# Kernel tuning notes

Measured on AMD Instinct MI355X. Metric: run time of the kernel, lower is better.

Reference implementation:

```python
import jax, jax.numpy as jnp
import numpy as np
from jax.scipy.special import logsumexp

DIM_N, DIM_E, DIM_U = 64, 128, 64
MID, A = 32, 16
N_PER, B = 12, 128  # 128 fully-connected graphs of 12 nodes


def _lin_params(k, fin, fout):
    k1, k2 = jax.random.split(k)
    lim = 1.0 / np.sqrt(fin)
    W = jax.random.uniform(k1, (fin, fout), minval=-lim, maxval=lim)
    b = jax.random.uniform(k2, (fout,), minval=-lim, maxval=lim)
    return W, b


def setup_inputs() -> dict:
    key = jax.random.key(0)
    ks = jax.random.split(key, 12)
    # fully connected directed graph (no self loops), per component
    s, d = np.meshgrid(np.arange(N_PER), np.arange(N_PER), indexing='ij')
    m = s != d
    s1, d1 = s[m].astype(np.int64), d[m].astype(np.int64)
    Epg = s1.size  # 132
    M = np.zeros((N_PER, N_PER), np.int64)
    M[s1, d1] = np.arange(Epg)
    rev1 = M[d1, s1]
    noff = (np.arange(B, dtype=np.int64) * N_PER)[:, None]
    eoff = (np.arange(B, dtype=np.int64) * Epg)[:, None]
    src = jnp.asarray((s1[None] + noff).reshape(-1))
    dst = jnp.asarray((d1[None] + noff).reshape(-1))
    idx_revs = jnp.asarray((rev1[None] + eoff).reshape(-1))
    E, Nt = B * Epg, B * N_PER
    edge_feats = jax.random.normal(ks[0], (E, DIM_E))
    node_feats = jax.random.normal(ks[1], (Nt, DIM_N))
    graph_feats = jax.random.normal(ks[2], (B, DIM_U))
    edge_feat_reflected = edge_feats[idx_revs]
    u = jax.random.uniform(ks[3], (E, 2), minval=1e-6, maxval=1.0)
    gumbel_noise = -jnp.log(-jnp.log(u))
    W_jf, b_jf = _lin_params(ks[4], DIM_E + DIM_U, A * MID)
    W_if, b_if = _lin_params(ks[5], DIM_N + DIM_U, A)
    W_ju, b_ju = _lin_params(ks[6], DIM_E + DIM_U, A * MID)
    W_iu, b_iu = _lin_params(ks[7], DIM_N + DIM_U, A)
    W_fl, b_fl = _lin_params(ks[8], DIM_E + DIM_U, MID)
    W_cls, b_cls = _lin_params(ks[9], MID, 2)
    return dict(edge_feats=edge_feats, node_feats=node_feats, graph_feats=graph_feats,
                edge_feat_reflected=edge_feat_reflected, src=src, dst=dst, idx_revs=idx_revs,
                gumbel_noise=gumbel_noise, W_jf=W_jf, b_jf=b_jf, W_if=W_if, b_if=b_if,
                W_ju=W_ju, b_ju=b_ju, W_iu=W_iu, b_iu=b_iu, W_fl=W_fl, b_fl=b_fl,
                W_cls=W_cls, b_cls=b_cls)


def reference(edge_feats, node_feats, graph_feats, edge_feat_reflected, src, dst, idx_revs,
              gumbel_noise, W_jf, b_jf, W_if, b_if, W_ju, b_ju, W_iu, b_iu,
              W_fl, b_fl, W_cls, b_cls):
    Bn = graph_feats.shape[0]
    Nt = node_feats.shape[0]
    E = edge_feats.shape[0]
    npg = Nt // Bn          # nodes per graph == number of BP iterations
    epg = E // Bn
    a = b_if.shape[0]       # num_acts
    mid = W_cls.shape[0]    # mid_pair

    # broadcast graph-level features to edges / nodes
    u_e = jnp.repeat(graph_feats, epg, axis=0)   # [E, du]
    u_n = jnp.repeat(graph_feats, npg, axis=0)   # [Nt, du]

    xe = jnp.concatenate([edge_feats, u_e], axis=-1)
    xer = jnp.concatenate([edge_feat_reflected, u_e], axis=-1)
    xn = jnp.concatenate([node_feats, u_n], axis=-1)

    indiv_factor = xn @ W_if + b_if      # [Nt, A]
    indiv_util = xn @ W_iu + b_iu        # [Nt, A]

    fc = (xe @ W_jf + b_jf).reshape(E, a, mid)
    fcr = (xer @ W_jf + b_jf).reshape(E, a, mid)
    factor_vals = jnp.einsum('eam,ebm->eab', fc, fcr)   # [E, A, A]
    uc = (xe @ W_ju + b_ju).reshape(E, a, mid)
    ucr = (xer @ W_ju + b_ju).reshape(E, a, mid)
    util_vals = jnp.einsum('eam,ebm->eab', uc, ucr)     # [E, A, A]

    # hard gumbel-softmax edge gating; noise shared with reverse edge
    flag_repr = (xe @ W_fl + b_fl) * (xer @ W_fl + b_fl)
    logits = flag_repr @ W_cls + b_cls                  # [E, 2]
    eid = jnp.arange(E)
    noise = gumbel_noise[jnp.minimum(eid, idx_revs)]
    y_soft = jax.nn.softmax(logits + noise, axis=-1)
    y_hard = jax.nn.one_hot(jnp.argmax(y_soft, axis=-1), 2, dtype=y_soft.dtype)
    flags = y_soft + jax.lax.stop_gradient(y_hard - y_soft)
    flag0 = flags[:, 0][:, None]                        # [E, 1]

    fvT = factor_vals.transpose(0, 2, 1)
    uvT = util_vals.transpose(0, 2, 1)
    if_src, if_dst = indiv_factor[src], indiv_factor[dst]
    iu_src, iu_dst = indiv_util[src], indiv_util[dst]

    def step(carry, _):
        mm_n, um_n, msg_e, rmsg_e, umsg_e, rumsg_e = carry
        agg = mm_n[src] - rmsg_e + if_src                      # [E, A]
        m = factor_vals + agg[:, None, :]                      # [E, A, A]
        m_sum = jax.nn.log_softmax(logsumexp(m, axis=-1), axis=-1)
        new_msg = m_sum * flag0
        agg_rev = mm_n[dst] - msg_e + if_dst
        m_rev = fvT + agg_rev[:, None, :]
        m_rev_sum = jax.nn.log_softmax(logsumexp(m_rev, axis=-1), axis=-1)
        new_rmsg = m_rev_sum * flag0
        util = um_n[src] - rumsg_e + iu_src
        new_umsg = ((util_vals + util[:, None, :]) * jax.nn.softmax(m, axis=-1)).sum(-1) * flag0
        rev_util = um_n[dst] - umsg_e + iu_dst
        new_rumsg = ((uvT + rev_util[:, None, :]) * jax.nn.softmax(m_rev, axis=-1)).sum(-1) * flag0
        new_mm_n = jax.ops.segment_sum(new_msg, dst, num_segments=Nt)
        new_um_n = jax.ops.segment_sum(new_umsg, dst, num_segments=Nt)
        return (new_mm_n, new_um_n, new_msg, new_rmsg, new_umsg, new_rumsg), None

    zn = jnp.zeros((Nt, a), edge_feats.dtype)
    ze = jnp.zeros((E, a), edge_feats.dtype)
    carry0 = (zn, zn, ze, ze, ze, ze)
    (mm_n, um_n, _, _, _, _), _ = jax.lax.scan(step, carry0, None, length=npg)

    node0 = jnp.arange(Bn) * npg
    return (um_n + indiv_util)[node0]   # [B, A]
```

## Files before the change

kernel.cpp:

```cpp
#include <hip/hip_runtime.h>
#include <hip/hip_bf16.h>

typedef unsigned short ushort_t;
typedef __bf16 bf16x8 __attribute__((ext_vector_type(8)));
typedef float f32x4 __attribute__((ext_vector_type(4)));

#define E_TOT 16896
#define NT    1536
#define BGR   128
#define NPG   12
#define EPG   132
#define KD    192
#define KD2   576
#define NJ    512
#define ADIM  16
#define MIDD  32
#define NCAN  8448

#if defined(__has_builtin)
#  if __has_builtin(__builtin_amdgcn_global_load_lds)
#    define HAS_GLL 1
#  else
#    define HAS_GLL 0
#  endif
#else
#  define HAS_GLL 0
#endif

#if HAS_GLL
__device__ __forceinline__ void gll16(const ushort_t* g, ushort_t* s) {
    __builtin_amdgcn_global_load_lds(
        (const __attribute__((address_space(1))) unsigned int*)g,
        (__attribute__((address_space(3))) unsigned int*)s, 16, 0, 0);
}
#endif

__device__ __forceinline__ float b2f(ushort_t u) {
    union { float f; unsigned int i; } c; c.i = ((unsigned int)u) << 16; return c.f;
}
__device__ __forceinline__ ushort_t f2b(float f) {
    union { float f; unsigned int i; } c; c.f = f;
    unsigned int i = c.i;
    unsigned int r = (i + 0x7FFFu + ((i >> 16) & 1u)) >> 16;
    return (ushort_t)r;
}
__device__ __forceinline__ int rev_local(int i) {
    int s = i / 11;
    int p = i - 11 * s;
    int d = p + (p >= s ? 1 : 0);
    return d * 11 + (s < d ? s : s - 1);
}

__global__ __launch_bounds__(256) void prep_kernel(
    const float* __restrict__ Wjf, const float* __restrict__ Wju,
    const float* __restrict__ ef,  const float* __restrict__ gf,
    ushort_t* __restrict__ WtJFs, ushort_t* __restrict__ WtJUs,
    ushort_t* __restrict__ XeS)
{
    int idx = blockIdx.x * 256 + threadIdx.x;
    const int T1 = NJ * KD;
    if (idx < T1) {
        int n = idx / KD, k = idx - n * KD;
        float wf = Wjf[k * NJ + n];
        ushort_t hf = f2b(wf);
        WtJFs[n * KD2 + k]       = hf;
        WtJFs[n * KD2 + 192 + k] = hf;
        WtJFs[n * KD2 + 384 + k] = f2b(wf - b2f(hf));
        float wu = Wju[k * NJ + n];
        ushort_t hu = f2b(wu);
        WtJUs[n * KD2 + k]       = hu;
        WtJUs[n * KD2 + 192 + k] = hu;
        WtJUs[n * KD2 + 384 + k] = f2b(wu - b2f(hu));
        return;
    }
    idx -= T1;
    if (idx < E_TOT * KD) {
        int e = idx / KD, k = idx - e * KD;
        float x = (k < 128) ? ef[(size_t)e * 128 + k] : gf[(e / EPG) * 64 + (k - 128)];
        ushort_t h = f2b(x);
        XeS[(size_t)e * KD2 + k]       = h;
        XeS[(size_t)e * KD2 + 192 + k] = f2b(x - b2f(h));
        XeS[(size_t)e * KD2 + 384 + k] = h;
    }
}

__global__ __launch_bounds__(256) void gemm_kernel(
    const ushort_t* __restrict__ X, const ushort_t* __restrict__ Wt,
    const float* __restrict__ bias, float* __restrict__ H)
{
    __shared__ ushort_t As[2][128][32];
    __shared__ ushort_t Bs[2][128][32];
    int tid = threadIdx.x, lane = tid & 63, w = tid >> 6;
    int m0 = blockIdx.y * 128, n0 = blockIdx.x * 128;
    int wm = (w >> 1) * 64, wn = (w & 1) * 64;
    int r = lane & 15, q = lane >> 4;
    f32x4 acc[4][4] = {};

    int sr = w * 32 + (lane >> 2);
    int sc = (lane & 3) * 8;
    const ushort_t* xg0 = X  + (size_t)(m0 + sr)      * KD2 + sc;
    const ushort_t* xg1 = X  + (size_t)(m0 + sr + 16) * KD2 + sc;
    const ushort_t* wg0 = Wt + (size_t)(n0 + sr)      * KD2 + sc;
    const ushort_t* wg1 = Wt + (size_t)(n0 + sr + 16) * KD2 + sc;

#if HAS_GLL
    auto stage = [&](int p, int kk) {
        gll16(xg0 + kk, &As[p][w * 32][0]);
        gll16(xg1 + kk, &As[p][w * 32 + 16][0]);
        gll16(wg0 + kk, &Bs[p][w * 32][0]);
        gll16(wg1 + kk, &Bs[p][w * 32 + 16][0]);
    };
#else
    auto stage = [&](int p, int kk) {
        uint4 a0 = *(const uint4*)(xg0 + kk);
        uint4 a1 = *(const uint4*)(xg1 + kk);
        uint4 b0 = *(const uint4*)(wg0 + kk);
        uint4 b1 = *(const uint4*)(wg1 + kk);
        *(uint4*)&As[p][sr][sc]      = a0;
        *(uint4*)&As[p][sr + 16][sc] = a1;
        *(uint4*)&Bs[p][sr][sc]      = b0;
        *(uint4*)&Bs[p][sr + 16][sc] = b1;
    };
#endif

    stage(0, 0);
    int cur = 0;
    for (int kk = 0; kk < KD2; kk += 32) {
        __syncthreads();
        if (kk + 32 < KD2) stage(cur ^ 1, kk + 32);
        bf16x8 af[4], bf[4];
#pragma unroll
        for (int mi = 0; mi < 4; ++mi)
            af[mi] = *(const bf16x8*)&As[cur][wm + mi * 16 + r][q * 8];
#pragma unroll
        for (int ni = 0; ni < 4; ++ni)
            bf[ni] = *(const bf16x8*)&Bs[cur][wn + ni * 16 + r][q * 8];
#pragma unroll
        for (int mi = 0; mi < 4; ++mi)
#pragma unroll
            for (int ni = 0; ni < 4; ++ni)
                acc[mi][ni] = __builtin_amdgcn_mfma_f32_16x16x32_bf16(
                    af[mi], bf[ni], acc[mi][ni], 0, 0, 0);
        cur ^= 1;
    }
#pragma unroll
    for (int ni = 0; ni < 4; ++ni) {
        int col = n0 + wn + ni * 16 + r;
        float bvf = bias[col];
#pragma unroll
        for (int mi = 0; mi < 4; ++mi) {
            int rowb = m0 + wm + mi * 16 + q * 4;
            float* dst = H + (size_t)rowb * NJ + col;
#pragma unroll
            for (int rr = 0; rr < 4; ++rr)
                dst[(size_t)rr * NJ] = acc[mi][ni][rr] + bvf;
        }
    }
}

__global__ __launch_bounds__(256) void pair_kernel(
    const float* __restrict__ H, float* __restrict__ OutV)
{
    __shared__ float sA[4][16][36];
    __shared__ float sB[4][16][36];
    __shared__ float sC[4][16][20];
    int tid = threadIdx.x, w = tid >> 6, lane = tid & 63;
    int c = blockIdx.x * 4 + w;
    int gg = c / 66, cl = c - gg * 66;
    int s = 0;
    while (cl >= 11 - s) { cl -= 11 - s; ++s; }
    int d = s + 1 + cl;
    int e  = gg * EPG + s * 11 + (d - 1);
    int re = gg * EPG + d * 11 + s;
    const float* hA = H + (size_t)e * NJ;
    const float* hB = H + (size_t)re * NJ;
    int a = lane >> 2, mseg = (lane & 3) * 8;
    float4 va0 = *(const float4*)(hA + a * 32 + mseg);
    float4 va1 = *(const float4*)(hA + a * 32 + mseg + 4);
    float4 vb0 = *(const float4*)(hB + a * 32 + mseg);
    float4 vb1 = *(const float4*)(hB + a * 32 + mseg + 4);
    *(float4*)&sA[w][a][mseg]     = va0;
    *(float4*)&sA[w][a][mseg + 4] = va1;
    *(float4*)&sB[w][a][mseg]     = vb0;
    *(float4*)&sB[w][a][mseg + 4] = vb1;
    __syncthreads();

    int b = lane & 15, a0 = (lane >> 4) * 4;
    float4 ac0 = {0,0,0,0}, ac1 = {0,0,0,0}, ac2 = {0,0,0,0}, ac3 = {0,0,0,0};
#pragma unroll
    for (int m4 = 0; m4 < 8; ++m4) {
        float4 vb = *(const float4*)&sB[w][b][m4 * 4];
        float4 x0 = *(const float4*)&sA[w][a0 + 0][m4 * 4];
        float4 x1 = *(const float4*)&sA[w][a0 + 1][m4 * 4];
        float4 x2 = *(const float4*)&sA[w][a0 + 2][m4 * 4];
        float4 x3 = *(const float4*)&sA[w][a0 + 3][m4 * 4];
        ac0.x += x0.x * vb.x; ac0.y += x0.y * vb.y; ac0.z += x0.z * vb.z; ac0.w += x0.w * vb.w;
        ac1.x += x1.x * vb.x; ac1.y += x1.y * vb.y; ac1.z += x1.z * vb.z; ac1.w += x1.w * vb.w;
        ac2.x += x2.x * vb.x; ac2.y += x2.y * vb.y; ac2.z += x2.z * vb.z; ac2.w += x2.w * vb.w;
        ac3.x += x3.x * vb.x; ac3.y += x3.y * vb.y; ac3.z += x3.z * vb.z; ac3.w += x3.w * vb.w;
    }
    float v0 = ac0.x + ac0.y + ac0.z + ac0.w;
    float v1 = ac1.x + ac1.y + ac1.z + ac1.w;
    float v2 = ac2.x + ac2.y + ac2.z + ac2.w;
    float v3 = ac3.x + ac3.y + ac3.z + ac3.w;
    float* oe = OutV + (size_t)e * 256;
    oe[(a0 + 0) * 16 + b] = v0;
    oe[(a0 + 1) * 16 + b] = v1;
    oe[(a0 + 2) * 16 + b] = v2;
    oe[(a0 + 3) * 16 + b] = v3;
    sC[w][b][a0 + 0] = v0;
    sC[w][b][a0 + 1] = v1;
    sC[w][b][a0 + 2] = v2;
    sC[w][b][a0 + 3] = v3;
    __syncthreads();
    int rr = lane >> 2, cc = (lane & 3) * 4;
    float4 t4 = { sC[w][rr][cc], sC[w][rr][cc + 1], sC[w][rr][cc + 2], sC[w][rr][cc + 3] };
    *(float4*)(OutV + (size_t)re * 256 + lane * 4) = t4;
}

__global__ __launch_bounds__(256) void hfl_kernel(
    const float* __restrict__ ef, const float* __restrict__ gf,
    const float* __restrict__ Wfl, const float* __restrict__ bfl,
    float* __restrict__ HFL)
{
    __shared__ float Ws[KD][32];
    __shared__ float xr[64][KD];
    int tid = threadIdx.x;
    int e0 = blockIdx.x * 64;
    for (int i = tid; i < KD * 32; i += 256) Ws[i >> 5][i & 31] = Wfl[i];
    for (int i4 = tid; i4 < 64 * 48; i4 += 256) {
        int slot = i4 / 48, kq = i4 - slot * 48;
        int e = e0 + slot;
        float4 v;
        if (kq < 32) v = *(const float4*)&ef[(size_t)e * 128 + kq * 4];
        else         v = *(const float4*)&gf[(e / EPG) * 64 + (kq - 32) * 4];
        *(float4*)&xr[slot][kq * 4] = v;
    }
    __syncthreads();
    int j = tid & 31, es = tid >> 5;
    float acc[8];
#pragma unroll
    for (int i = 0; i < 8; ++i) acc[i] = bfl[j];
    for (int k = 0; k < KD; k += 4) {
        float w0 = Ws[k][j], w1 = Ws[k + 1][j], w2 = Ws[k + 2][j], w3 = Ws[k + 3][j];
#pragma unroll
        for (int i = 0; i < 8; ++i) {
            float4 x4 = *(const float4*)&xr[es + 8 * i][k];
            acc[i] += x4.x * w0; acc[i] += x4.y * w1;
            acc[i] += x4.z * w2; acc[i] += x4.w * w3;
        }
    }
#pragma unroll
    for (int i = 0; i < 8; ++i)
        HFL[(size_t)(e0 + es + 8 * i) * 32 + j] = acc[i];
}

__global__ __launch_bounds__(256) void node_kernel(
    const float* __restrict__ nf, const float* __restrict__ gf,
    const float* __restrict__ Wif, const float* __restrict__ bif,
    const float* __restrict__ Wiu, const float* __restrict__ biu,
    float* __restrict__ IFF, float* __restrict__ IUU)
{
    __shared__ float Ws[128 * 32];
    __shared__ float xr[8][128];
    int tid = threadIdx.x;
    int n0 = blockIdx.x * 8;
    for (int i = tid; i < 128 * 32; i += 256) {
        int k = i >> 5, j = i & 31;
        Ws[i] = (j < 16) ? Wif[k * 16 + j] : Wiu[k * 16 + (j - 16)];
    }
    for (int i = tid; i < 8 * 128; i += 256) {
        int slot = i >> 7, k = i & 127;
        int n = n0 + slot;
        xr[slot][k] = (k < 64) ? nf[(size_t)n * 64 + k] : gf[(n / NPG) * 64 + (k - 64)];
    }
    __syncthreads();
    int slot = tid >> 5, j = tid & 31;
    float acc = (j < 16) ? bif[j] : biu[j - 16];
#pragma unroll 8
    for (int k = 0; k < 128; ++k) acc += xr[slot][k] * Ws[k * 32 + j];
    int n = n0 + slot;
    if (j < 16) IFF[n * 16 + j] = acc;
    else        IUU[n * 16 + (j - 16)] = acc;
}

__global__ __launch_bounds__(256) void flags_kernel(
    const float* __restrict__ HFL,
    const float* __restrict__ Wcls, const float* __restrict__ bcls,
    const float* __restrict__ gum, float* __restrict__ FL)
{
    int e = blockIdx.x * 256 + threadIdx.x;
    if (e >= E_TOT) return;
    int g = e / EPG, li = e - g * EPG;
    int re = g * EPG + rev_local(li);
    float l0 = bcls[0], l1 = bcls[1];
    const float* ha = HFL + (size_t)e * 32;
    const float* hb = HFL + (size_t)re * 32;
#pragma unroll
    for (int j = 0; j < 32; ++j) {
        float p = ha[j] * hb[j];
        l0 += p * Wcls[j * 2 + 0];
        l1 += p * Wcls[j * 2 + 1];
    }
    int mn = min(e, re);
    l0 += gum[(size_t)mn * 2 + 0];
    l1 += gum[(size_t)mn * 2 + 1];
    FL[e] = (l0 >= l1) ? 1.0f : 0.0f;
}

__global__ __launch_bounds__(704, 3) void bp_kernel(
    const float* __restrict__ FV, const float* __restrict__ UV,
    const float* __restrict__ FL, const float* __restrict__ IFF,
    const float* __restrict__ IUU, float* __restrict__ out)
{
    int g = blockIdx.x, tid = threadIdx.x;
    __shared__ float msg[2][EPG][16];
    __shared__ float umsg[2][EPG][16];
    __shared__ float Asum[NPG][16], Usum[NPG][16];
    __shared__ float iffs[NPG][16], iuus[NPG][16];
    __shared__ float fls[EPG];

    for (int i = tid; i < 2 * EPG * 16; i += 704) {
        (&msg[0][0][0])[i] = 0.f;
        (&umsg[0][0][0])[i] = 0.f;
    }
    for (int i = tid; i < NPG * 16; i += 704) {
        float fi = IFF[g * NPG * 16 + i];
        float ui = IUU[g * NPG * 16 + i];
        (&iffs[0][0])[i] = fi; (&iuus[0][0])[i] = ui;
        (&Asum[0][0])[i] = fi; (&Usum[0][0])[i] = ui;
    }
    for (int i = tid; i < EPG; i += 704) fls[i] = FL[g * EPG + i];

    int w44 = tid >> 4, a = tid & 15;
    int sidx[3], ridx[3], eidx[3];
    float fv[3][16], uv[3][16], fle[3];
    const float* fvg = FV + (size_t)g * EPG * 256;
    const float* uvg = UV + (size_t)g * EPG * 256;
#pragma unroll
    for (int j = 0; j < 3; ++j) {
        int e = j * 44 + w44;
        eidx[j] = e;
        sidx[j] = e / 11;
        ridx[j] = rev_local(e);
        const float* fr = fvg + (size_t)e * 256 + a * 16;
        const float* ur = uvg + (size_t)e * 256 + a * 16;
#pragma unroll
        for (int q = 0; q < 4; ++q) {
            float4 f4 = *(const float4*)(fr + q * 4);
            float4 u4 = *(const float4*)(ur + q * 4);
            fv[j][q * 4 + 0] = f4.x; fv[j][q * 4 + 1] = f4.y;
            fv[j][q * 4 + 2] = f4.z; fv[j][q * 4 + 3] = f4.w;
            uv[j][q * 4 + 0] = u4.x; uv[j][q * 4 + 1] = u4.y;
            uv[j][q * 4 + 2] = u4.z; uv[j][q * 4 + 3] = u4.w;
        }
    }
    __syncthreads();
#pragma unroll
    for (int j = 0; j < 3; ++j) fle[j] = fls[eidx[j]];

    int cur = 0;
    for (int it = 0; it < NPG; ++it) {
        int nxt = cur ^ 1;
#pragma unroll
        for (int j = 0; j < 3; ++j) {
            int e = eidx[j], s = sidx[j], re = ridx[j];
            float t_m[16], t_u[16];
#pragma unroll
            for (int q = 0; q < 4; ++q) {
                float4 av  = *(const float4*)&Asum[s][q * 4];
                float4 mv  = *(const float4*)&msg[cur][re][q * 4];
                float4 usv = *(const float4*)&Usum[s][q * 4];
                float4 umv = *(const float4*)&umsg[cur][re][q * 4];
                t_m[q * 4 + 0] = fv[j][q * 4 + 0] + (av.x - mv.x);
                t_m[q * 4 + 1] = fv[j][q * 4 + 1] + (av.y - mv.y);
                t_m[q * 4 + 2] = fv[j][q * 4 + 2] + (av.z - mv.z);
                t_m[q * 4 + 3] = fv[j][q * 4 + 3] + (av.w - mv.w);
                t_u[q * 4 + 0] = uv[j][q * 4 + 0] + (usv.x - umv.x);
                t_u[q * 4 + 1] = uv[j][q * 4 + 1] + (usv.y - umv.y);
                t_u[q * 4 + 2] = uv[j][q * 4 + 2] + (usv.z - umv.z);
                t_u[q * 4 + 3] = uv[j][q * 4 + 3] + (usv.w - umv.w);
            }
            float mx = t_m[0];
#pragma unroll
            for (int b = 1; b < 16; ++b) mx = fmaxf(mx, t_m[b]);
            float S = 0.f, num = 0.f;
#pragma unroll
            for (int b = 0; b < 16; ++b) {
                float ev = __expf(t_m[b] - mx);
                S += ev;
                num += t_u[b] * ev;
            }
            float lse = mx + __logf(S);
            float unv = num / S;
            float M2 = lse;
            M2 = fmaxf(M2, __shfl_xor(M2, 1));
            M2 = fmaxf(M2, __shfl_xor(M2, 2));
            M2 = fmaxf(M2, __shfl_xor(M2, 4));
            M2 = fmaxf(M2, __shfl_xor(M2, 8));
            float se = __expf(lse - M2);
            se += __shfl_xor(se, 1);
            se += __shfl_xor(se, 2);
            se += __shfl_xor(se, 4);
            se += __shfl_xor(se, 8);
            float LSE = M2 + __logf(se);
            msg[nxt][e][a] = (lse - LSE) * fle[j];
            umsg[nxt][e][a] = unv * fle[j];
        }
        __syncthreads();
        if (tid < NPG * 16) {
            int n = tid >> 4, aa = tid & 15;
            float sm = 0.f, su = 0.f;
#pragma unroll
            for (int s = 0; s < NPG; ++s) {
                if (s == n) continue;
                int le = s * 11 + (n < s ? n : n - 1);
                sm += msg[nxt][le][aa];
                su += umsg[nxt][le][aa];
            }
            Asum[n][aa] = sm + iffs[n][aa];
            Usum[n][aa] = su + iuus[n][aa];
        }
        __syncthreads();
        cur = nxt;
    }
    if (tid < 16) {
        out[g * 16 + tid] = Usum[0][tid];
    }
}

extern "C" void kernel_launch(void* const* d_in, const int* in_sizes, int n_in,
                              void* d_out, int out_size, void* d_ws, size_t ws_size,
                              hipStream_t stream) {
    const float* edge_feats  = (const float*)d_in[0];
    const float* node_feats  = (const float*)d_in[1];
    const float* graph_feats = (const float*)d_in[2];
    const float* gumbel      = (const float*)d_in[7];
    const float* W_jf        = (const float*)d_in[8];
    const float* b_jf        = (const float*)d_in[9];
    const float* W_if        = (const float*)d_in[10];
    const float* b_if        = (const float*)d_in[11];
    const float* W_ju        = (const float*)d_in[12];
    const float* b_ju        = (const float*)d_in[13];
    const float* W_iu        = (const float*)d_in[14];
    const float* b_iu        = (const float*)d_in[15];
    const float* W_fl        = (const float*)d_in[16];
    const float* b_fl        = (const float*)d_in[17];
    const float* W_cls       = (const float*)d_in[18];
    const float* b_cls       = (const float*)d_in[19];
    float* out = (float*)d_out;
    (void)in_sizes; (void)n_in; (void)out_size; (void)ws_size;

    size_t off = 0;
    char* base = (char*)d_ws;
    auto alloc = [&](size_t bytes) {
        void* p = base + off;
        off += (bytes + 255) & ~(size_t)255;
        return p;
    };
    ushort_t* XeS   = (ushort_t*)alloc((size_t)E_TOT * KD2 * 2);
    ushort_t* WtJFs = (ushort_t*)alloc((size_t)NJ * KD2 * 2);
    ushort_t* WtJUs = (ushort_t*)alloc((size_t)NJ * KD2 * 2);
    float*    Hbuf  = (float*)   alloc((size_t)E_TOT * NJ * 4);
    float*    FVv   = (float*)   alloc((size_t)E_TOT * 256 * 4);
    float*    FLG   = (float*)   alloc((size_t)E_TOT * 4);
    float*    IFFp  = (float*)   alloc((size_t)NT * 16 * 4);
    float*    IUUp  = (float*)   alloc((size_t)NT * 16 * 4);
    float* HFL = Hbuf;
    float* UVv = (float*)XeS;

    const int prep_blocks = (NJ * KD + E_TOT * KD) / 256;
    prep_kernel<<<prep_blocks, 256, 0, stream>>>(W_jf, W_ju, edge_feats, graph_feats,
                                                 WtJFs, WtJUs, XeS);
    node_kernel<<<NT / 8, 256, 0, stream>>>(node_feats, graph_feats, W_if, b_if,
                                            W_iu, b_iu, IFFp, IUUp);
    hfl_kernel<<<E_TOT / 64, 256, 0, stream>>>(edge_feats, graph_feats, W_fl, b_fl, HFL);
    flags_kernel<<<E_TOT / 256, 256, 0, stream>>>(HFL, W_cls, b_cls, gumbel, FLG);
    gemm_kernel<<<dim3(NJ / 128, E_TOT / 128), 256, 0, stream>>>(XeS, WtJFs, b_jf, Hbuf);
    pair_kernel<<<NCAN / 4, 256, 0, stream>>>(Hbuf, FVv);
    gemm_kernel<<<dim3(NJ / 128, E_TOT / 128), 256, 0, stream>>>(XeS, WtJUs, b_ju, Hbuf);
    pair_kernel<<<NCAN / 4, 256, 0, stream>>>(Hbuf, UVv);
    bp_kernel<<<BGR, 704, 0, stream>>>(FVv, UVv, FLG, IFFp, IUUp, out);
}
```

Before: 247.5 us.

## Batch both factor GEMMs and pair passes via grid z, fold node and flag kernels into bp

Merges the two edge-factor GEMMs and the two pair transforms into single launches indexed by a grid z/y dimension, writing to separate H and FV/UV buffers when the workspace is large enough. The node linear layers and the Gumbel flag classifier are computed inside the belief-propagation kernel's prologue instead of in separate kernels. This cuts four kernel launches and gives the GEMM twice as many blocks for better occupancy. In exchange it needs a larger workspace, and the node matmul now runs serially per thread inside bp_kernel.

```diff
diff --git a/kernel.cpp b/kernel.cpp
--- a/kernel.cpp
+++ b/kernel.cpp
@@ -85,11 +85,18 @@
 }
 
 __global__ __launch_bounds__(256) void gemm_kernel(
-    const ushort_t* __restrict__ X, const ushort_t* __restrict__ Wt,
-    const float* __restrict__ bias, float* __restrict__ H)
+    const ushort_t* __restrict__ X,
+    const ushort_t* __restrict__ Wt0, const ushort_t* __restrict__ Wt1,
+    const float* __restrict__ b0, const float* __restrict__ b1,
+    float* __restrict__ Hbase)
 {
     __shared__ ushort_t As[2][128][32];
     __shared__ ushort_t Bs[2][128][32];
+    int z = blockIdx.z;
+    const ushort_t* Wt = z ? Wt1 : Wt0;
+    const float* bias = z ? b1 : b0;
+    float* H = Hbase + (size_t)z * E_TOT * NJ;
+
     int tid = threadIdx.x, lane = tid & 63, w = tid >> 6;
     int m0 = blockIdx.y * 128, n0 = blockIdx.x * 128;
     int wm = (w >> 1) * 64, wn = (w & 1) * 64;
@@ -114,12 +121,12 @@
     auto stage = [&](int p, int kk) {
         uint4 a0 = *(const uint4*)(xg0 + kk);
         uint4 a1 = *(const uint4*)(xg1 + kk);
-        uint4 b0 = *(const uint4*)(wg0 + kk);
-        uint4 b1 = *(const uint4*)(wg1 + kk);
+        uint4 bb0 = *(const uint4*)(wg0 + kk);
+        uint4 bb1 = *(const uint4*)(wg1 + kk);
         *(uint4*)&As[p][sr][sc]      = a0;
         *(uint4*)&As[p][sr + 16][sc] = a1;
-        *(uint4*)&Bs[p][sr][sc]      = b0;
-        *(uint4*)&Bs[p][sr + 16][sc] = b1;
+        *(uint4*)&Bs[p][sr][sc]      = bb0;
+        *(uint4*)&Bs[p][sr + 16][sc] = bb1;
     };
 #endif
 
@@ -159,11 +166,13 @@
 }
 
 __global__ __launch_bounds__(256) void pair_kernel(
-    const float* __restrict__ H, float* __restrict__ OutV)
+    const float* __restrict__ Hbase, float* __restrict__ Obase)
 {
     __shared__ float sA[4][16][36];
     __shared__ float sB[4][16][36];
     __shared__ float sC[4][16][20];
+    const float* H = Hbase + (size_t)blockIdx.y * E_TOT * NJ;
+    float* OutV = Obase + (size_t)blockIdx.y * E_TOT * 256;
     int tid = threadIdx.x, w = tid >> 6, lane = tid & 63;
     int c = blockIdx.x * 4 + w;
     int gg = c / 66, cl = c - gg * 66;
@@ -255,63 +264,14 @@
         HFL[(size_t)(e0 + es + 8 * i) * 32 + j] = acc[i];
 }
 
-__global__ __launch_bounds__(256) void node_kernel(
+__global__ __launch_bounds__(704, 3) void bp_kernel(
+    const float* __restrict__ FV, const float* __restrict__ UV,
+    const float* __restrict__ HFL, const float* __restrict__ Wcls,
+    const float* __restrict__ bcls, const float* __restrict__ gum,
     const float* __restrict__ nf, const float* __restrict__ gf,
     const float* __restrict__ Wif, const float* __restrict__ bif,
     const float* __restrict__ Wiu, const float* __restrict__ biu,
-    float* __restrict__ IFF, float* __restrict__ IUU)
-{
-    __shared__ float Ws[128 * 32];
-    __shared__ float xr[8][128];
-    int tid = threadIdx.x;
-    int n0 = blockIdx.x * 8;
-    for (int i = tid; i < 128 * 32; i += 256) {
-        int k = i >> 5, j = i & 31;
-        Ws[i] = (j < 16) ? Wif[k * 16 + j] : Wiu[k * 16 + (j - 16)];
-    }
-    for (int i = tid; i < 8 * 128; i += 256) {
-        int slot = i >> 7, k = i & 127;
-        int n = n0 + slot;
-        xr[slot][k] = (k < 64) ? nf[(size_t)n * 64 + k] : gf[(n / NPG) * 64 + (k - 64)];
-    }
-    __syncthreads();
-    int slot = tid >> 5, j = tid & 31;
-    float acc = (j < 16) ? bif[j] : biu[j - 16];
-#pragma unroll 8
-    for (int k = 0; k < 128; ++k) acc += xr[slot][k] * Ws[k * 32 + j];
-    int n = n0 + slot;
-    if (j < 16) IFF[n * 16 + j] = acc;
-    else        IUU[n * 16 + (j - 16)] = acc;
-}
-
-__global__ __launch_bounds__(256) void flags_kernel(
-    const float* __restrict__ HFL,
-    const float* __restrict__ Wcls, const float* __restrict__ bcls,
-    const float* __restrict__ gum, float* __restrict__ FL)
-{
-    int e = blockIdx.x * 256 + threadIdx.x;
-    if (e >= E_TOT) return;
-    int g = e / EPG, li = e - g * EPG;
-    int re = g * EPG + rev_local(li);
-    float l0 = bcls[0], l1 = bcls[1];
-    const float* ha = HFL + (size_t)e * 32;
-    const float* hb = HFL + (size_t)re * 32;
-#pragma unroll
-    for (int j = 0; j < 32; ++j) {
-        float p = ha[j] * hb[j];
-        l0 += p * Wcls[j * 2 + 0];
-        l1 += p * Wcls[j * 2 + 1];
-    }
-    int mn = min(e, re);
-    l0 += gum[(size_t)mn * 2 + 0];
-    l1 += gum[(size_t)mn * 2 + 1];
-    FL[e] = (l0 >= l1) ? 1.0f : 0.0f;
-}
-
-__global__ __launch_bounds__(704, 3) void bp_kernel(
-    const float* __restrict__ FV, const float* __restrict__ UV,
-    const float* __restrict__ FL, const float* __restrict__ IFF,
-    const float* __restrict__ IUU, float* __restrict__ out)
+    float* __restrict__ out)
 {
     int g = blockIdx.x, tid = threadIdx.x;
     __shared__ float msg[2][EPG][16];
@@ -324,13 +284,35 @@
         (&msg[0][0][0])[i] = 0.f;
         (&umsg[0][0][0])[i] = 0.f;
     }
-    for (int i = tid; i < NPG * 16; i += 704) {
-        float fi = IFF[g * NPG * 16 + i];
-        float ui = IUU[g * NPG * 16 + i];
-        (&iffs[0][0])[i] = fi; (&iuus[0][0])[i] = ui;
-        (&Asum[0][0])[i] = fi; (&Usum[0][0])[i] = ui;
-    }
-    for (int i = tid; i < EPG; i += 704) fls[i] = FL[g * EPG + i];
+    if (tid < NPG * 16) {
+        int nl = tid >> 4, aa = tid & 15;
+        int n = g * NPG + nl;
+        float accf = bif[aa], accu = biu[aa];
+        for (int k = 0; k < 128; ++k) {
+            float x = (k < 64) ? nf[(size_t)n * 64 + k] : gf[g * 64 + (k - 64)];
+            accf += x * Wif[k * 16 + aa];
+            accu += x * Wiu[k * 16 + aa];
+        }
+        iffs[nl][aa] = accf; iuus[nl][aa] = accu;
+        Asum[nl][aa] = accf; Usum[nl][aa] = accu;
+    }
+    if (tid < EPG) {
+        int el = tid, rel = rev_local(el);
+        int e = g * EPG + el, re = g * EPG + rel;
+        float l0 = bcls[0], l1 = bcls[1];
+        const float* ha = HFL + (size_t)e * 32;
+        const float* hb = HFL + (size_t)re * 32;
+#pragma unroll
+        for (int j = 0; j < 32; ++j) {
+            float p = ha[j] * hb[j];
+            l0 += p * Wcls[j * 2 + 0];
+            l1 += p * Wcls[j * 2 + 1];
+        }
+        int mn = min(e, re);
+        l0 += gum[(size_t)mn * 2 + 0];
+        l1 += gum[(size_t)mn * 2 + 1];
+        fls[el] = (l0 >= l1) ? 1.0f : 0.0f;
+    }
 
     int w44 = tid >> 4, a = tid & 15;
     int sidx[3], ridx[3], eidx[3];
@@ -449,7 +431,7 @@
     const float* W_cls       = (const float*)d_in[18];
     const float* b_cls       = (const float*)d_in[19];
     float* out = (float*)d_out;
-    (void)in_sizes; (void)n_in; (void)out_size; (void)ws_size;
+    (void)in_sizes; (void)n_in; (void)out_size;
 
     size_t off = 0;
     char* base = (char*)d_ws;
@@ -461,24 +443,40 @@
     ushort_t* XeS   = (ushort_t*)alloc((size_t)E_TOT * KD2 * 2);
     ushort_t* WtJFs = (ushort_t*)alloc((size_t)NJ * KD2 * 2);
     ushort_t* WtJUs = (ushort_t*)alloc((size_t)NJ * KD2 * 2);
-    float*    Hbuf  = (float*)   alloc((size_t)E_TOT * NJ * 4);
-    float*    FVv   = (float*)   alloc((size_t)E_TOT * 256 * 4);
-    float*    FLG   = (float*)   alloc((size_t)E_TOT * 4);
-    float*    IFFp  = (float*)   alloc((size_t)NT * 16 * 4);
-    float*    IUUp  = (float*)   alloc((size_t)NT * 16 * 4);
-    float* HFL = Hbuf;
-    float* UVv = (float*)XeS;
-
+    float*    HFL   = (float*)   alloc((size_t)E_TOT * 32 * 4);
+
+    const size_t fused_need = off + (size_t)E_TOT * NJ * 2 * 4
+                                  + (size_t)E_TOT * 512 * 4
+                                  + 4096;
     const int prep_blocks = (NJ * KD + E_TOT * KD) / 256;
+
     prep_kernel<<<prep_blocks, 256, 0, stream>>>(W_jf, W_ju, edge_feats, graph_feats,
                                                  WtJFs, WtJUs, XeS);
-    node_kernel<<<NT / 8, 256, 0, stream>>>(node_feats, graph_feats, W_if, b_if,
-                                            W_iu, b_iu, IFFp, IUUp);
     hfl_kernel<<<E_TOT / 64, 256, 0, stream>>>(edge_feats, graph_feats, W_fl, b_fl, HFL);
-    flags_kernel<<<E_TOT / 256, 256, 0, stream>>>(HFL, W_cls, b_cls, gumbel, FLG);
-    gemm_kernel<<<dim3(NJ / 128, E_TOT / 128), 256, 0, stream>>>(XeS, WtJFs, b_jf, Hbuf);
-    pair_kernel<<<NCAN / 4, 256, 0, stream>>>(Hbuf, FVv);
-    gemm_kernel<<<dim3(NJ / 128, E_TOT / 128), 256, 0, stream>>>(XeS, WtJUs, b_ju, Hbuf);
-    pair_kernel<<<NCAN / 4, 256, 0, stream>>>(Hbuf, UVv);
-    bp_kernel<<<BGR, 704, 0, stream>>>(FVv, UVv, FLG, IFFp, IUUp, out);
-}
+
+    if (ws_size >= fused_need) {
+        float* H2   = (float*)alloc((size_t)E_TOT * NJ * 2 * 4);
+        float* FVUV = (float*)alloc((size_t)E_TOT * 512 * 4);
+        float* FVv = FVUV;
+        float* UVv = FVUV + (size_t)E_TOT * 256;
+        gemm_kernel<<<dim3(NJ / 128, E_TOT / 128, 2), 256, 0, stream>>>(
+            XeS, WtJFs, WtJUs, b_jf, b_ju, H2);
+        pair_kernel<<<dim3(NCAN / 4, 2), 256, 0, stream>>>(H2, FVUV);
+        bp_kernel<<<BGR, 704, 0, stream>>>(FVv, UVv, HFL, W_cls, b_cls, gumbel,
+                                           node_feats, graph_feats,
+                                           W_if, b_if, W_iu, b_iu, out);
+    } else {
+        float* Hbuf = (float*)alloc((size_t)E_TOT * NJ * 4);
+        float* FVv  = (float*)alloc((size_t)E_TOT * 256 * 4);
+        float* UVv  = (float*)XeS;
+        gemm_kernel<<<dim3(NJ / 128, E_TOT / 128, 1), 256, 0, stream>>>(
+            XeS, WtJFs, WtJFs, b_jf, b_jf, Hbuf);
+        pair_kernel<<<dim3(NCAN / 4, 1), 256, 0, stream>>>(Hbuf, FVv);
+        gemm_kernel<<<dim3(NJ / 128, E_TOT / 128, 1), 256, 0, stream>>>(
+            XeS, WtJUs, WtJUs, b_ju, b_ju, Hbuf);
+        pair_kernel<<<dim3(NCAN / 4, 1), 256, 0, stream>>>(Hbuf, UVv);
+        bp_kernel<<<BGR, 704, 0, stream>>>(FVv, UVv, HFL, W_cls, b_cls, gumbel,
+                                           node_feats, graph_feats,
+                                           W_if, b_if, W_iu, b_iu, out);
+    }
+}
```

After: 240.7 us. 1.03x faster.

## Fuse GEMM with pair contraction and fold node/flag kernels into neighbors

Applied to the files above, without the earlier changes.

The two big GEMMs and their pair contractions are merged into one kernel. Each block computes the full 512-wide H rows for 16 edge/reverse-edge pairs in shared memory and contracts them directly, so the large fp32 H intermediate never goes through global memory. The node projection is folded into the prep kernel as extra blocks, and the flag computation is moved into the BP kernel prologue, removing three launches. The cost is that each block now streams the whole weight matrix for only 32 rows, which cuts B-operand reuse, and the shared-memory footprint is larger, which may reduce occupancy.

```diff
diff --git a/kernel.cpp b/kernel.cpp
--- a/kernel.cpp
+++ b/kernel.cpp
@@ -13,9 +13,8 @@
 #define KD    192
 #define KD2   576
 #define NJ    512
-#define ADIM  16
-#define MIDD  32
 #define NCAN  8448
+#define PPB   16
 
 #if defined(__has_builtin)
 #  if __has_builtin(__builtin_amdgcn_global_load_lds)
@@ -50,76 +49,130 @@
     int d = p + (p >= s ? 1 : 0);
     return d * 11 + (s < d ? s : s - 1);
 }
+__device__ __forceinline__ void canon_decode(int c, int& e, int& re) {
+    int g = c / 66, cl = c - g * 66;
+    int s = 0;
+    while (cl >= 11 - s) { cl -= 11 - s; ++s; }
+    int d = s + 1 + cl;
+    e  = g * EPG + s * 11 + (d - 1);
+    re = g * EPG + d * 11 + s;
+}
 
 __global__ __launch_bounds__(256) void prep_kernel(
     const float* __restrict__ Wjf, const float* __restrict__ Wju,
     const float* __restrict__ ef,  const float* __restrict__ gf,
+    const float* __restrict__ nf,
+    const float* __restrict__ Wif, const float* __restrict__ bif,
+    const float* __restrict__ Wiu, const float* __restrict__ biu,
     ushort_t* __restrict__ WtJFs, ushort_t* __restrict__ WtJUs,
-    ushort_t* __restrict__ XeS)
+    ushort_t* __restrict__ XeS,
+    float* __restrict__ IFF, float* __restrict__ IUU)
 {
-    int idx = blockIdx.x * 256 + threadIdx.x;
+    __shared__ float Ws[128 * 32];
+    __shared__ float xr[8][128];
     const int T1 = NJ * KD;
-    if (idx < T1) {
-        int n = idx / KD, k = idx - n * KD;
-        float wf = Wjf[k * NJ + n];
-        ushort_t hf = f2b(wf);
-        WtJFs[n * KD2 + k]       = hf;
-        WtJFs[n * KD2 + 192 + k] = hf;
-        WtJFs[n * KD2 + 384 + k] = f2b(wf - b2f(hf));
-        float wu = Wju[k * NJ + n];
-        ushort_t hu = f2b(wu);
-        WtJUs[n * KD2 + k]       = hu;
-        WtJUs[n * KD2 + 192 + k] = hu;
-        WtJUs[n * KD2 + 384 + k] = f2b(wu - b2f(hu));
-        return;
-    }
-    idx -= T1;
-    if (idx < E_TOT * KD) {
+    const int NBE = (T1 + E_TOT * KD) / 256;
+    if (blockIdx.x < (unsigned)NBE) {
+        int idx = blockIdx.x * 256 + threadIdx.x;
+        if (idx < T1) {
+            int n = idx / KD, k = idx - n * KD;
+            float wf = Wjf[k * NJ + n];
+            ushort_t hf = f2b(wf);
+            WtJFs[n * KD2 + k]       = hf;
+            WtJFs[n * KD2 + 192 + k] = hf;
+            WtJFs[n * KD2 + 384 + k] = f2b(wf - b2f(hf));
+            float wu = Wju[k * NJ + n];
+            ushort_t hu = f2b(wu);
+            WtJUs[n * KD2 + k]       = hu;
+            WtJUs[n * KD2 + 192 + k] = hu;
+            WtJUs[n * KD2 + 384 + k] = f2b(wu - b2f(hu));
+            return;
+        }
+        idx -= T1;
         int e = idx / KD, k = idx - e * KD;
         float x = (k < 128) ? ef[(size_t)e * 128 + k] : gf[(e / EPG) * 64 + (k - 128)];
         ushort_t h = f2b(x);
         XeS[(size_t)e * KD2 + k]       = h;
         XeS[(size_t)e * KD2 + 192 + k] = f2b(x - b2f(h));
         XeS[(size_t)e * KD2 + 384 + k] = h;
-    }
-}
-
-__global__ __launch_bounds__(256) void gemm_kernel(
-    const ushort_t* __restrict__ X, const ushort_t* __restrict__ Wt,
-    const float* __restrict__ bias, float* __restrict__ H)
+        return;
+    }
+    int tid = threadIdx.x;
+    int n0 = (blockIdx.x - NBE) * 8;
+    for (int i = tid; i < 128 * 32; i += 256) {
+        int k = i >> 5, j = i & 31;
+        Ws[i] = (j < 16) ? Wif[k * 16 + j] : Wiu[k * 16 + (j - 16)];
+    }
+    for (int i = tid; i < 8 * 128; i += 256) {
+        int slot = i >> 7, k = i & 127;
+        int n = n0 + slot;
+        xr[slot][k] = (k < 64) ? nf[(size_t)n * 64 + k] : gf[(n / NPG) * 64 + (k - 64)];
+    }
+    __syncthreads();
+    int slot = tid >> 5, j = tid & 31;
+    float acc = (j < 16) ? bif[j] : biu[j - 16];
+#pragma unroll 8
+    for (int k = 0; k < 128; ++k) acc += xr[slot][k] * Ws[k * 32 + j];
+    int n = n0 + slot;
+    if (j < 16) IFF[n * 16 + j] = acc;
+    else        IUU[n * 16 + (j - 16)] = acc;
+}
+
+__global__ __launch_bounds__(256) void gemmpair_kernel(
+    const ushort_t* __restrict__ XeS,
+    const ushort_t* __restrict__ Wt0, const ushort_t* __restrict__ Wt1,
+    const float* __restrict__ b0, const float* __restrict__ b1,
+    float* __restrict__ Obase)
 {
-    __shared__ ushort_t As[2][128][32];
-    __shared__ ushort_t Bs[2][128][32];
+    __shared__ union {
+        struct {
+            ushort_t Bs[2][512][32];
+            ushort_t As[2][32][32];
+        } st;
+        float Hs[32][16][33];
+    } u;
+    int z = blockIdx.y;
+    const ushort_t* Wt = z ? Wt1 : Wt0;
+    const float* bias = z ? b1 : b0;
+    float* OutV = Obase + (size_t)z * E_TOT * 256;
+
     int tid = threadIdx.x, lane = tid & 63, w = tid >> 6;
-    int m0 = blockIdx.y * 128, n0 = blockIdx.x * 128;
-    int wm = (w >> 1) * 64, wn = (w & 1) * 64;
+    int brow = lane >> 2;
+    int bseg = (lane & 3) * 8;
     int r = lane & 15, q = lane >> 4;
-    f32x4 acc[4][4] = {};
-
-    int sr = w * 32 + (lane >> 2);
-    int sc = (lane & 3) * 8;
-    const ushort_t* xg0 = X  + (size_t)(m0 + sr)      * KD2 + sc;
-    const ushort_t* xg1 = X  + (size_t)(m0 + sr + 16) * KD2 + sc;
-    const ushort_t* wg0 = Wt + (size_t)(n0 + sr)      * KD2 + sc;
-    const ushort_t* wg1 = Wt + (size_t)(n0 + sr + 16) * KD2 + sc;
+
+    int arow = w * 16 + brow;
+    int ae = 0;
+    {
+        int ee, rr;
+        canon_decode(blockIdx.x * PPB + (arow & 15), ee, rr);
+        ae = (arow < 16) ? ee : rr;
+    }
+    const ushort_t* agp = XeS + (size_t)ae * KD2 + bseg;
+
+    f32x4 acc[2][8] = {};
 
 #if HAS_GLL
-    auto stage = [&](int p, int kk) {
-        gll16(xg0 + kk, &As[p][w * 32][0]);
-        gll16(xg1 + kk, &As[p][w * 32 + 16][0]);
-        gll16(wg0 + kk, &Bs[p][w * 32][0]);
-        gll16(wg1 + kk, &Bs[p][w * 32 + 16][0]);
+    auto stage = [&](int pb, int kk) {
+#pragma unroll
+        for (int i = 0; i < 8; ++i) {
+            int n = w * 128 + i * 16 + brow;
+            gll16(Wt + (size_t)n * KD2 + kk + bseg, &u.st.Bs[pb][w * 128 + i * 16][0]);
+        }
+        if (w < 2) gll16(agp + kk, &u.st.As[pb][w * 16][0]);
     };
 #else
-    auto stage = [&](int p, int kk) {
-        uint4 a0 = *(const uint4*)(xg0 + kk);
-        uint4 a1 = *(const uint4*)(xg1 + kk);
-        uint4 b0 = *(const uint4*)(wg0 + kk);
-        uint4 b1 = *(const uint4*)(wg1 + kk);
-        *(uint4*)&As[p][sr][sc]      = a0;
-        *(uint4*)&As[p][sr + 16][sc] = a1;
-        *(uint4*)&Bs[p][sr][sc]      = b0;
-        *(uint4*)&Bs[p][sr + 16][sc] = b1;
+    auto stage = [&](int pb, int kk) {
+#pragma unroll
+        for (int i = 0; i < 8; ++i) {
+            int n = w * 128 + i * 16 + brow;
+            uint4 v = *(const uint4*)(Wt + (size_t)n * KD2 + kk + bseg);
+            *(uint4*)&u.st.Bs[pb][n][bseg] = v;
+        }
+        if (w < 2) {
+            uint4 v = *(const uint4*)(agp + kk);
+            *(uint4*)&u.st.As[pb][arow][bseg] = v;
+        }
     };
 #endif
 
@@ -128,94 +181,61 @@
     for (int kk = 0; kk < KD2; kk += 32) {
         __syncthreads();
         if (kk + 32 < KD2) stage(cur ^ 1, kk + 32);
-        bf16x8 af[4], bf[4];
-#pragma unroll
-        for (int mi = 0; mi < 4; ++mi)
-            af[mi] = *(const bf16x8*)&As[cur][wm + mi * 16 + r][q * 8];
-#pragma unroll
-        for (int ni = 0; ni < 4; ++ni)
-            bf[ni] = *(const bf16x8*)&Bs[cur][wn + ni * 16 + r][q * 8];
-#pragma unroll
-        for (int mi = 0; mi < 4; ++mi)
-#pragma unroll
-            for (int ni = 0; ni < 4; ++ni)
-                acc[mi][ni] = __builtin_amdgcn_mfma_f32_16x16x32_bf16(
-                    af[mi], bf[ni], acc[mi][ni], 0, 0, 0);
+        bf16x8 af0 = *(const bf16x8*)&u.st.As[cur][r][q * 8];
+        bf16x8 af1 = *(const bf16x8*)&u.st.As[cur][16 + r][q * 8];
+#pragma unroll
+        for (int t = 0; t < 8; ++t) {
+            bf16x8 bf = *(const bf16x8*)&u.st.Bs[cur][w * 128 + t * 16 + r][q * 8];
+            acc[0][t] = __builtin_amdgcn_mfma_f32_16x16x32_bf16(af0, bf, acc[0][t], 0, 0, 0);
+            acc[1][t] = __builtin_amdgcn_mfma_f32_16x16x32_bf16(af1, bf, acc[1][t], 0, 0, 0);
+        }
         cur ^= 1;
     }
-#pragma unroll
-    for (int ni = 0; ni < 4; ++ni) {
-        int col = n0 + wn + ni * 16 + r;
+    __syncthreads();
+
+#pragma unroll
+    for (int t = 0; t < 8; ++t) {
+        int col = w * 128 + t * 16 + r;
         float bvf = bias[col];
-#pragma unroll
-        for (int mi = 0; mi < 4; ++mi) {
-            int rowb = m0 + wm + mi * 16 + q * 4;
-            float* dst = H + (size_t)rowb * NJ + col;
+        int ca = col >> 5, cm = col & 31;
+#pragma unroll
+        for (int mi = 0; mi < 2; ++mi) {
+            int row = mi * 16 + q * 4;
 #pragma unroll
             for (int rr = 0; rr < 4; ++rr)
-                dst[(size_t)rr * NJ] = acc[mi][ni][rr] + bvf;
-        }
-    }
-}
-
-__global__ __launch_bounds__(256) void pair_kernel(
-    const float* __restrict__ H, float* __restrict__ OutV)
-{
-    __shared__ float sA[4][16][36];
-    __shared__ float sB[4][16][36];
-    __shared__ float sC[4][16][20];
-    int tid = threadIdx.x, w = tid >> 6, lane = tid & 63;
-    int c = blockIdx.x * 4 + w;
-    int gg = c / 66, cl = c - gg * 66;
-    int s = 0;
-    while (cl >= 11 - s) { cl -= 11 - s; ++s; }
-    int d = s + 1 + cl;
-    int e  = gg * EPG + s * 11 + (d - 1);
-    int re = gg * EPG + d * 11 + s;
-    const float* hA = H + (size_t)e * NJ;
-    const float* hB = H + (size_t)re * NJ;
-    int a = lane >> 2, mseg = (lane & 3) * 8;
-    float4 va0 = *(const float4*)(hA + a * 32 + mseg);
-    float4 va1 = *(const float4*)(hA + a * 32 + mseg + 4);
-    float4 vb0 = *(const float4*)(hB + a * 32 + mseg);
-    float4 vb1 = *(const float4*)(hB + a * 32 + mseg + 4);
-    *(float4*)&sA[w][a][mseg]     = va0;
-    *(float4*)&sA[w][a][mseg + 4] = va1;
-    *(float4*)&sB[w][a][mseg]     = vb0;
-    *(float4*)&sB[w][a][mseg + 4] = vb1;
+                u.Hs[row + rr][ca][cm] = acc[mi][t][rr] + bvf;
+        }
+    }
     __syncthreads();
 
-    int b = lane & 15, a0 = (lane >> 4) * 4;
-    float4 ac0 = {0,0,0,0}, ac1 = {0,0,0,0}, ac2 = {0,0,0,0}, ac3 = {0,0,0,0};
+    int p = tid >> 4, a = tid & 15;
+    int e, re;
+    canon_decode(blockIdx.x * PPB + p, e, re);
+    float av[32];
 #pragma unroll
     for (int m4 = 0; m4 < 8; ++m4) {
-        float4 vb = *(const float4*)&sB[w][b][m4 * 4];
-        float4 x0 = *(const float4*)&sA[w][a0 + 0][m4 * 4];
-        float4 x1 = *(const float4*)&sA[w][a0 + 1][m4 * 4];
-        float4 x2 = *(const float4*)&sA[w][a0 + 2][m4 * 4];
-        float4 x3 = *(const float4*)&sA[w][a0 + 3][m4 * 4];
-        ac0.x += x0.x * vb.x; ac0.y += x0.y * vb.y; ac0.z += x0.z * vb.z; ac0.w += x0.w * vb.w;
-        ac1.x += x1.x * vb.x; ac1.y += x1.y * vb.y; ac1.z += x1.z * vb.z; ac1.w += x1.w * vb.w;
-        ac2.x += x2.x * vb.x; ac2.y += x2.y * vb.y; ac2.z += x2.z * vb.z; ac2.w += x2.w * vb.w;
-        ac3.x += x3.x * vb.x; ac3.y += x3.y * vb.y; ac3.z += x3.z * vb.z; ac3.w += x3.w * vb.w;
-    }
-    float v0 = ac0.x + ac0.y + ac0.z + ac0.w;
-    float v1 = ac1.x + ac1.y + ac1.z + ac1.w;
-    float v2 = ac2.x + ac2.y + ac2.z + ac2.w;
-    float v3 = ac3.x + ac3.y + ac3.z + ac3.w;
-    float* oe = OutV + (size_t)e * 256;
-    oe[(a0 + 0) * 16 + b] = v0;
-    oe[(a0 + 1) * 16 + b] = v1;
-    oe[(a0 + 2) * 16 + b] = v2;
-    oe[(a0 + 3) * 16 + b] = v3;
-    sC[w][b][a0 + 0] = v0;
-    sC[w][b][a0 + 1] = v1;
-    sC[w][b][a0 + 2] = v2;
-    sC[w][b][a0 + 3] = v3;
-    __syncthreads();
-    int rr = lane >> 2, cc = (lane & 3) * 4;
-    float4 t4 = { sC[w][rr][cc], sC[w][rr][cc + 1], sC[w][rr][cc + 2], sC[w][rr][cc + 3] };
-    *(float4*)(OutV + (size_t)re * 256 + lane * 4) = t4;
+        float4 v = *(const float4*)&u.Hs[p][a][m4 * 4];
+        av[m4 * 4 + 0] = v.x; av[m4 * 4 + 1] = v.y;
+        av[m4 * 4 + 2] = v.z; av[m4 * 4 + 3] = v.w;
+    }
+    float outv[16];
+#pragma unroll
+    for (int b = 0; b < 16; ++b) {
+        float s0 = 0, s1 = 0, s2 = 0, s3 = 0;
+#pragma unroll
+        for (int m4 = 0; m4 < 8; ++m4) {
+            float4 bv = *(const float4*)&u.Hs[16 + p][b][m4 * 4];
+            s0 += av[m4 * 4 + 0] * bv.x; s1 += av[m4 * 4 + 1] * bv.y;
+            s2 += av[m4 * 4 + 2] * bv.z; s3 += av[m4 * 4 + 3] * bv.w;
+        }
+        outv[b] = (s0 + s1) + (s2 + s3);
+    }
+    float* oe = OutV + (size_t)e * 256 + a * 16;
+#pragma unroll
+    for (int b = 0; b < 16; ++b) oe[b] = outv[b];
+    float* orr = OutV + (size_t)re * 256 + a;
+#pragma unroll
+    for (int b = 0; b < 16; ++b) orr[b * 16] = outv[b];
 }
 
 __global__ __launch_bounds__(256) void hfl_kernel(
@@ -255,63 +275,12 @@
         HFL[(size_t)(e0 + es + 8 * i) * 32 + j] = acc[i];
 }
 
-__global__ __launch_bounds__(256) void node_kernel(
-    const float* __restrict__ nf, const float* __restrict__ gf,
-    const float* __restrict__ Wif, const float* __restrict__ bif,
-    const float* __restrict__ Wiu, const float* __restrict__ biu,
-    float* __restrict__ IFF, float* __restrict__ IUU)
-{
-    __shared__ float Ws[128 * 32];
-    __shared__ float xr[8][128];
-    int tid = threadIdx.x;
-    int n0 = blockIdx.x * 8;
-    for (int i = tid; i < 128 * 32; i += 256) {
-        int k = i >> 5, j = i & 31;
-        Ws[i] = (j < 16) ? Wif[k * 16 + j] : Wiu[k * 16 + (j - 16)];
-    }
-    for (int i = tid; i < 8 * 128; i += 256) {
-        int slot = i >> 7, k = i & 127;
-        int n = n0 + slot;
-        xr[slot][k] = (k < 64) ? nf[(size_t)n * 64 + k] : gf[(n / NPG) * 64 + (k - 64)];
-    }
-    __syncthreads();
-    int slot = tid >> 5, j = tid & 31;
-    float acc = (j < 16) ? bif[j] : biu[j - 16];
-#pragma unroll 8
-    for (int k = 0; k < 128; ++k) acc += xr[slot][k] * Ws[k * 32 + j];
-    int n = n0 + slot;
-    if (j < 16) IFF[n * 16 + j] = acc;
-    else        IUU[n * 16 + (j - 16)] = acc;
-}
-
-__global__ __launch_bounds__(256) void flags_kernel(
-    const float* __restrict__ HFL,
-    const float* __restrict__ Wcls, const float* __restrict__ bcls,
-    const float* __restrict__ gum, float* __restrict__ FL)
-{
-    int e = blockIdx.x * 256 + threadIdx.x;
-    if (e >= E_TOT) return;
-    int g = e / EPG, li = e - g * EPG;
-    int re = g * EPG + rev_local(li);
-    float l0 = bcls[0], l1 = bcls[1];
-    const float* ha = HFL + (size_t)e * 32;
-    const float* hb = HFL + (size_t)re * 32;
-#pragma unroll
-    for (int j = 0; j < 32; ++j) {
-        float p = ha[j] * hb[j];
-        l0 += p * Wcls[j * 2 + 0];
-        l1 += p * Wcls[j * 2 + 1];
-    }
-    int mn = min(e, re);
-    l0 += gum[(size_t)mn * 2 + 0];
-    l1 += gum[(size_t)mn * 2 + 1];
-    FL[e] = (l0 >= l1) ? 1.0f : 0.0f;
-}
-
 __global__ __launch_bounds__(704, 3) void bp_kernel(
     const float* __restrict__ FV, const float* __restrict__ UV,
-    const float* __restrict__ FL, const float* __restrict__ IFF,
-    const float* __restrict__ IUU, float* __restrict__ out)
+    const float* __restrict__ HFL, const float* __restrict__ Wcls,
+    const float* __restrict__ bcls, const float* __restrict__ gum,
+    const float* __restrict__ IFF, const float* __restrict__ IUU,
+    float* __restrict__ out)
 {
     int g = blockIdx.x, tid = threadIdx.x;
     __shared__ float msg[2][EPG][16];
@@ -324,13 +293,29 @@
         (&msg[0][0][0])[i] = 0.f;
         (&umsg[0][0][0])[i] = 0.f;
     }
-    for (int i = tid; i < NPG * 16; i += 704) {
-        float fi = IFF[g * NPG * 16 + i];
-        float ui = IUU[g * NPG * 16 + i];
-        (&iffs[0][0])[i] = fi; (&iuus[0][0])[i] = ui;
-        (&Asum[0][0])[i] = fi; (&Usum[0][0])[i] = ui;
-    }
-    for (int i = tid; i < EPG; i += 704) fls[i] = FL[g * EPG + i];
+    if (tid < NPG * 16) {
+        float fi = IFF[g * NPG * 16 + tid];
+        float ui = IUU[g * NPG * 16 + tid];
+        (&iffs[0][0])[tid] = fi; (&iuus[0][0])[tid] = ui;
+        (&Asum[0][0])[tid] = fi; (&Usum[0][0])[tid] = ui;
+    }
+    if (tid < EPG) {
+        int el = tid, rel = rev_local(el);
+        int e = g * EPG + el, re = g * EPG + rel;
+        float l0 = bcls[0], l1 = bcls[1];
+        const float* ha = HFL + (size_t)e * 32;
+        const float* hb = HFL + (size_t)re * 32;
+#pragma unroll
+        for (int j = 0; j < 32; ++j) {
+            float pp = ha[j] * hb[j];
+            l0 += pp * Wcls[j * 2 + 0];
+            l1 += pp * Wcls[j * 2 + 1];
+        }
+        int mn = min(e, re);
+        l0 += gum[(size_t)mn * 2 + 0];
+        l1 += gum[(size_t)mn * 2 + 1];
+        fls[el] = (l0 >= l1) ? 1.0f : 0.0f;
+    }
 
     int w44 = tid >> 4, a = tid & 15;
     int sidx[3], ridx[3], eidx[3];
@@ -346,13 +331,13 @@
         const float* fr = fvg + (size_t)e * 256 + a * 16;
         const float* ur = uvg + (size_t)e * 256 + a * 16;
 #pragma unroll
-        for (int q = 0; q < 4; ++q) {
-            float4 f4 = *(const float4*)(fr + q * 4);
-            float4 u4 = *(const float4*)(ur + q * 4);
-            fv[j][q * 4 + 0] = f4.x; fv[j][q * 4 + 1] = f4.y;
-            fv[j][q * 4 + 2] = f4.z; fv[j][q * 4 + 3] = f4.w;
-            uv[j][q * 4 + 0] = u4.x; uv[j][q * 4 + 1] = u4.y;
-            uv[j][q * 4 + 2] = u4.z; uv[j][q * 4 + 3] = u4.w;
+        for (int qq = 0; qq < 4; ++qq) {
+            float4 f4 = *(const float4*)(fr + qq * 4);
+            float4 u4 = *(const float4*)(ur + qq * 4);
+            fv[j][qq * 4 + 0] = f4.x; fv[j][qq * 4 + 1] = f4.y;
+            fv[j][qq * 4 + 2] = f4.z; fv[j][qq * 4 + 3] = f4.w;
+            uv[j][qq * 4 + 0] = u4.x; uv[j][qq * 4 + 1] = u4.y;
+            uv[j][qq * 4 + 2] = u4.z; uv[j][qq * 4 + 3] = u4.w;
         }
     }
     __syncthreads();
@@ -367,19 +352,19 @@
             int e = eidx[j], s = sidx[j], re = ridx[j];
             float t_m[16], t_u[16];
 #pragma unroll
-            for (int q = 0; q < 4; ++q) {
-                float4 av  = *(const float4*)&Asum[s][q * 4];
-                float4 mv  = *(const float4*)&msg[cur][re][q * 4];
-                float4 usv = *(const float4*)&Usum[s][q * 4];
-                float4 umv = *(const float4*)&umsg[cur][re][q * 4];
-                t_m[q * 4 + 0] = fv[j][q * 4 + 0] + (av.x - mv.x);
-                t_m[q * 4 + 1] = fv[j][q * 4 + 1] + (av.y - mv.y);
-                t_m[q * 4 + 2] = fv[j][q * 4 + 2] + (av.z - mv.z);
-                t_m[q * 4 + 3] = fv[j][q * 4 + 3] + (av.w - mv.w);
-                t_u[q * 4 + 0] = uv[j][q * 4 + 0] + (usv.x - umv.x);
-                t_u[q * 4 + 1] = uv[j][q * 4 + 1] + (usv.y - umv.y);
-                t_u[q * 4 + 2] = uv[j][q * 4 + 2] + (usv.z - umv.z);
-                t_u[q * 4 + 3] = uv[j][q * 4 + 3] + (usv.w - umv.w);
+            for (int qq = 0; qq < 4; ++qq) {
+                float4 av  = *(const float4*)&Asum[s][qq * 4];
+                float4 mv  = *(const float4*)&msg[cur][re][qq * 4];
+                float4 usv = *(const float4*)&Usum[s][qq * 4];
+                float4 umv = *(const float4*)&umsg[cur][re][qq * 4];
+                t_m[qq * 4 + 0] = fv[j][qq * 4 + 0] + (av.x - mv.x);
+                t_m[qq * 4 + 1] = fv[j][qq * 4 + 1] + (av.y - mv.y);
+                t_m[qq * 4 + 2] = fv[j][qq * 4 + 2] + (av.z - mv.z);
+                t_m[qq * 4 + 3] = fv[j][qq * 4 + 3] + (av.w - mv.w);
+                t_u[qq * 4 + 0] = uv[j][qq * 4 + 0] + (usv.x - umv.x);
+                t_u[qq * 4 + 1] = uv[j][qq * 4 + 1] + (usv.y - umv.y);
+                t_u[qq * 4 + 2] = uv[j][qq * 4 + 2] + (usv.z - umv.z);
+                t_u[qq * 4 + 3] = uv[j][qq * 4 + 3] + (usv.w - umv.w);
             }
             float mx = t_m[0];
 #pragma unroll
@@ -461,24 +446,22 @@
     ushort_t* XeS   = (ushort_t*)alloc((size_t)E_TOT * KD2 * 2);
     ushort_t* WtJFs = (ushort_t*)alloc((size_t)NJ * KD2 * 2);
     ushort_t* WtJUs = (ushort_t*)alloc((size_t)NJ * KD2 * 2);
-    float*    Hbuf  = (float*)   alloc((size_t)E_TOT * NJ * 4);
-    float*    FVv   = (float*)   alloc((size_t)E_TOT * 256 * 4);
-    float*    FLG   = (float*)   alloc((size_t)E_TOT * 4);
+    float*    HFL   = (float*)   alloc((size_t)E_TOT * 32 * 4);
     float*    IFFp  = (float*)   alloc((size_t)NT * 16 * 4);
     float*    IUUp  = (float*)   alloc((size_t)NT * 16 * 4);
-    float* HFL = Hbuf;
-    float* UVv = (float*)XeS;
-
-    const int prep_blocks = (NJ * KD + E_TOT * KD) / 256;
-    prep_kernel<<<prep_blocks, 256, 0, stream>>>(W_jf, W_ju, edge_feats, graph_feats,
-                                                 WtJFs, WtJUs, XeS);
-    node_kernel<<<NT / 8, 256, 0, stream>>>(node_feats, graph_feats, W_if, b_if,
-                                            W_iu, b_iu, IFFp, IUUp);
+    float*    FVUV  = (float*)   alloc((size_t)E_TOT * 512 * 4);
+    float* FVv = FVUV;
+    float* UVv = FVUV + (size_t)E_TOT * 256;
+
+    const int NBE = (NJ * KD + E_TOT * KD) / 256;
+    const int prep_blocks = NBE + NT / 8;
+
+    prep_kernel<<<prep_blocks, 256, 0, stream>>>(
+        W_jf, W_ju, edge_feats, graph_feats, node_feats,
+        W_if, b_if, W_iu, b_iu, WtJFs, WtJUs, XeS, IFFp, IUUp);
     hfl_kernel<<<E_TOT / 64, 256, 0, stream>>>(edge_feats, graph_feats, W_fl, b_fl, HFL);
-    flags_kernel<<<E_TOT / 256, 256, 0, stream>>>(HFL, W_cls, b_cls, gumbel, FLG);
-    gemm_kernel<<<dim3(NJ / 128, E_TOT / 128), 256, 0, stream>>>(XeS, WtJFs, b_jf, Hbuf);
-    pair_kernel<<<NCAN / 4, 256, 0, stream>>>(Hbuf, FVv);
-    gemm_kernel<<<dim3(NJ / 128, E_TOT / 128), 256, 0, stream>>>(XeS, WtJUs, b_ju, Hbuf);
-    pair_kernel<<<NCAN / 4, 256, 0, stream>>>(Hbuf, UVv);
-    bp_kernel<<<BGR, 704, 0, stream>>>(FVv, UVv, FLG, IFFp, IUUp, out);
-}
+    gemmpair_kernel<<<dim3(NCAN / PPB, 2), 256, 0, stream>>>(
+        XeS, WtJFs, WtJUs, b_jf, b_ju, FVUV);
+    bp_kernel<<<BGR, 704, 0, stream>>>(FVv, UVv, HFL, W_cls, b_cls, gumbel,
+                                       IFFp, IUUp, out);
+}
```

After: 353.4 us. +42.8%, slower.
